# Optimization experiments

Measured on AMD Instinct MI355X. Metric: run time of the kernel, lower is better.

The kernel has to match this reference:

```python
import jax, jax.numpy as jnp
import numpy as np
from jax import lax

THRESHOLD = 0.95
NUM_HEADS = 32
Q_HEAD_DIM = 96
K_DIM = 1024
EPS = 1e-8


def dynamic_token_replacement(emb, thr=THRESHOLD):
    """Greedy sequential merge: token j is replaced by the first earlier
    *unused* token i with cosine sim > thr. emb: (S, D) -> (S, D)."""
    S = emb.shape[0]
    norm = jnp.maximum(jnp.linalg.norm(emb, axis=-1, keepdims=True), EPS)
    n = emb / norm
    sim = n @ n.T  # (S, S) cosine similarity
    idx = jnp.arange(S)

    def step(carry, xs):
        used, rep = carry
        i, row = xs
        # i can only absorb later, unused tokens, and only if i itself is unused
        cand = (idx > i) & (row > thr) & (~used) & (~used[i])
        rep = jnp.where(cand, i, rep)
        used = used | cand
        return (used, rep), None

    (used, rep), _ = lax.scan(step, (jnp.zeros(S, bool), idx), (idx, sim))
    return emb[rep]


def setup_inputs() -> dict:
    key = jax.random.key(0)
    ks = jax.random.split(key, 7)
    B, S, D = 2, 1024, 3072
    s = 0.02
    return {
        "hidden_states": jax.random.normal(ks[0], (B, S, D), jnp.float32),
        "Wq": jax.random.normal(ks[1], (D, D), jnp.float32) * s,
        "bq": jnp.zeros((D,), jnp.float32),
        "Wk": jax.random.normal(ks[2], (D, K_DIM), jnp.float32) * s,
        "bk": jnp.zeros((K_DIM,), jnp.float32),
        "Wv": jax.random.normal(ks[3], (D, K_DIM), jnp.float32) * s,
        "bv": jnp.zeros((K_DIM,), jnp.float32),
        "Wqk": jax.random.normal(ks[4], (Q_HEAD_DIM, K_DIM), jnp.float32) * s,
        "bqk": jnp.zeros((K_DIM,), jnp.float32),
        "Wo": jax.random.normal(ks[5], (K_DIM, D), jnp.float32) * s,
        "bo": jnp.zeros((D,), jnp.float32),
    }


def reference(hidden_states, Wq, bq, Wk, bk, Wv, bv, Wqk, bqk, Wo, bo):
    B, S, D = hidden_states.shape
    q = hidden_states @ Wq + bq                      # (B, S, 3072)
    k = hidden_states @ Wk + bk                      # (B, S, 1024)
    v = hidden_states @ Wv + bv                      # (B, S, 1024)

    q = q.reshape(B, S, NUM_HEADS, Q_HEAD_DIM).transpose(0, 2, 1, 3)  # (B, H, S, 96)
    q_new = q @ Wqk + bqk                            # (B, H, S, 1024)

    new_k = jax.vmap(dynamic_token_replacement)(k)   # (B, S, 1024)
    new_v = jax.vmap(dynamic_token_replacement)(v)   # (B, S, 1024)

    scale = 1.0 / jnp.sqrt(jnp.float32(K_DIM))
    scores = jnp.einsum('bhsk,btk->bhst', q_new, new_k) * scale  # (B, H, S, S)
    attn = jax.nn.softmax(scores, axis=-1)
    out = jnp.einsum('bhst,btk->bhsk', attn, new_v)  # (B, H, S, 1024)
    out = out.mean(axis=1)                           # (B, S, 1024)
    return out @ Wo + bo                             # (B, S, 3072)
```

## Files before the change

kernel.cpp:

```cpp
#include <hip/hip_runtime.h>
#include <hip/hip_bf16.h>
#include <stdint.h>

#define BATCH 2
#define SEQ   1024
#define DIM   3072
#define KDIM  1024
#define NHEAD 32
#define HDQ   96
#define THR_SIM 0.95f

typedef unsigned short u16;
typedef __attribute__((ext_vector_type(8))) short short8;
typedef __attribute__((ext_vector_type(4))) float f32x4;

typedef const __attribute__((address_space(1))) unsigned int* gas_ptr;
typedef __attribute__((address_space(3))) unsigned int* las_ptr;

__device__ __forceinline__ void glds16(const u16* g, u16* l) {
  __builtin_amdgcn_global_load_lds((gas_ptr)g, (las_ptr)l, 16, 0, 0);
}

__device__ __forceinline__ u16 f2bf(float f) {
  union { float f; unsigned u; } v; v.f = f;
  unsigned r = v.u + 0x7FFFu + ((v.u >> 16) & 1u);
  return (u16)(r >> 16);
}
__device__ __forceinline__ float bf2f(u16 x) {
  union { unsigned u; float f; } v; v.u = ((unsigned)x) << 16; return v.f;
}

__device__ __forceinline__ f32x4 mfma16(short8 a, short8 b, f32x4 c) {
  return __builtin_amdgcn_mfma_f32_16x16x32_bf16(a, b, c, 0, 0, 0);
}

__global__ void k_cvt_bf16(const float* __restrict__ in, u16* __restrict__ out, int n4) {
  int i = blockIdx.x * blockDim.x + threadIdx.x;
  if (i < n4) {
    float4 v = ((const float4*)in)[i];
    ushort4 o;
    o.x = f2bf(v.x); o.y = f2bf(v.y); o.z = f2bf(v.z); o.w = f2bf(v.w);
    ((ushort4*)out)[i] = o;
  }
}

__global__ void k_tr_f32_bf16(const float* __restrict__ in, u16* __restrict__ out, int R, int C) {
  __shared__ float t[32][33];
  int c0 = blockIdx.x * 32, r0 = blockIdx.y * 32;
  int tx = threadIdx.x, ty = threadIdx.y;
  #pragma unroll
  for (int k = 0; k < 4; ++k)
    t[ty + 8 * k][tx] = in[(size_t)(r0 + ty + 8 * k) * C + c0 + tx];
  __syncthreads();
  #pragma unroll
  for (int k = 0; k < 4; ++k)
    out[(size_t)(c0 + ty + 8 * k) * R + r0 + tx] = f2bf(t[tx][ty + 8 * k]);
}

__global__ void k_tr_bf16(const u16* __restrict__ in, u16* __restrict__ out,
                          int ldin, int ldout, long long zsIn, long long zsOut) {
  __shared__ u16 t[32][33];
  const u16* ib = in + (size_t)blockIdx.z * zsIn;
  u16* ob = out + (size_t)blockIdx.z * zsOut;
  int c0 = blockIdx.x * 32, r0 = blockIdx.y * 32;
  int tx = threadIdx.x, ty = threadIdx.y;
  #pragma unroll
  for (int k = 0; k < 4; ++k)
    t[ty + 8 * k][tx] = ib[(size_t)(r0 + ty + 8 * k) * ldin + c0 + tx];
  __syncthreads();
  #pragma unroll
  for (int k = 0; k < 4; ++k)
    ob[(size_t)(c0 + ty + 8 * k) * ldout + r0 + tx] = t[tx][ty + 8 * k];
}

__global__ void k_build_wqke(const float* __restrict__ Wqk, const float* __restrict__ bqk,
                             u16* __restrict__ out) {
  const int n = blockIdx.x;
  const int c = threadIdx.x * 4;
  float4 v;
  if (n < 96)       v = *(const float4*)(Wqk + (size_t)n * KDIM + c);
  else if (n == 96) v = *(const float4*)(bqk + c);
  else              v = make_float4(0.f, 0.f, 0.f, 0.f);
  ushort4 o;
  o.x = f2bf(v.x); o.y = f2bf(v.y); o.z = f2bf(v.z); o.w = f2bf(v.w);
  *(ushort4*)(out + (size_t)n * KDIM + c) = o;
}

__global__ void k_bkv(const float* __restrict__ bk, const float* __restrict__ bv,
                      float* __restrict__ out) {
  int i = blockIdx.x * 256 + threadIdx.x;
  if (i < 2048) out[i] = (i < 1024) ? bk[i] : bv[i - 1024];
}

template<bool OUT_BF16, bool BIAS>
__global__ __launch_bounds__(256, 4) void k_gemm_bt(
    const u16* __restrict__ A, const u16* __restrict__ Bt, void* __restrict__ Cv,
    const float* __restrict__ bias, int M, int N, int K,
    int lda, int ldb, int ldc,
    long long bsAH, long long bsAL, long long bsBH, long long bsBL,
    long long bsCH, long long bsCL)
{
  const int zb = blockIdx.y, zH = zb >> 1, zL = zb & 1;
  A  += (size_t)(zH * bsAH + zL * bsAL);
  Bt += (size_t)(zH * bsBH + zL * bsBL);
  u16*   Cb16 = (u16*)Cv + (size_t)(zH * bsCH + zL * bsCL);
  float* Cf32 = (float*)Cv + (size_t)(zH * bsCH + zL * bsCL);

  __shared__ u16 As[2][128 * 32];
  __shared__ u16 Bs[2][64 * 32];
  const int nt = N >> 6;
  const int tm = blockIdx.x / nt, tn = blockIdx.x % nt;
  const int tid = threadIdx.x, lane = tid & 63, wid = tid >> 6;
  const int wr = wid >> 1, wc = wid & 1, li = lane & 15, lg = lane >> 4;

  const int srow = tid >> 2;
  const int scol = (((tid & 3) ^ ((srow >> 1) & 3)) << 3);
  const u16* gA0 = A + (size_t)(tm * 128 + srow) * lda + scol;
  const u16* gA1 = gA0 + (size_t)64 * lda;
  const u16* gB0 = Bt + (size_t)(tn * 64 + srow) * ldb + scol;
  const int wof = wid * 512;

  f32x4 acc[4][2];
  #pragma unroll
  for (int a = 0; a < 4; ++a)
    #pragma unroll
    for (int b = 0; b < 2; ++b) acc[a][b] = (f32x4){0.f, 0.f, 0.f, 0.f};

  const int sl = (lg ^ ((li >> 1) & 3)) * 8;

  const int nk = K >> 5;
  glds16(gA0, As[0] + wof);
  glds16(gA1, As[0] + 2048 + wof);
  glds16(gB0, Bs[0] + wof);
  __syncthreads();

  int cur = 0;
  for (int kt = 0; kt < nk; ++kt) {
    if (kt + 1 < nk) {
      const int k0 = (kt + 1) << 5;
      glds16(gA0 + k0, As[cur ^ 1] + wof);
      glds16(gA1 + k0, As[cur ^ 1] + 2048 + wof);
      glds16(gB0 + k0, Bs[cur ^ 1] + wof);
    }
    short8 af[4], bfv[2];
    #pragma unroll
    for (int mf = 0; mf < 4; ++mf)
      af[mf] = *(const short8*)(As[cur] + (wr * 64 + mf * 16 + li) * 32 + sl);
    #pragma unroll
    for (int nf = 0; nf < 2; ++nf)
      bfv[nf] = *(const short8*)(Bs[cur] + (wc * 32 + nf * 16 + li) * 32 + sl);
    #pragma unroll
    for (int mf = 0; mf < 4; ++mf)
      #pragma unroll
      for (int nf = 0; nf < 2; ++nf)
        acc[mf][nf] = mfma16(af[mf], bfv[nf], acc[mf][nf]);
    __syncthreads();
    cur ^= 1;
  }
  #pragma unroll
  for (int mf = 0; mf < 4; ++mf) {
    #pragma unroll
    for (int nf = 0; nf < 2; ++nf) {
      const int col = tn * 64 + wc * 32 + nf * 16 + li;
      const float bb = BIAS ? bias[col] : 0.f;
      #pragma unroll
      for (int j = 0; j < 4; ++j) {
        const int row = tm * 128 + wr * 64 + mf * 16 + lg * 4 + j;
        const float v = acc[mf][nf][j] + bb;
        if (OUT_BF16) Cb16[(size_t)row * ldc + col] = f2bf(v);
        else          Cf32[(size_t)row * ldc + col] = v;
      }
    }
  }
}

__global__ void k_norms(const float* __restrict__ gram, float* __restrict__ nrm,
                        int* __restrict__ anyCnt) {
  const int s = blockIdx.x, j = threadIdx.x;
  const float* g = gram + (size_t)s * SEQ * SEQ;
  float nj = fmaxf(sqrtf(fmaxf(g[(size_t)j * SEQ + j], 0.f)), 1e-8f);
  nrm[s * SEQ + j] = nj;
  if (j == 0) anyCnt[s] = 0;
}

__global__ void k_rowany(const float* __restrict__ gram, const float* __restrict__ nrm,
                         unsigned char* __restrict__ rowAny, int* __restrict__ anyCnt) {
  const int i = blockIdx.x, s = blockIdx.y, t = threadIdx.x;
  const float* g = gram + (size_t)s * SEQ * SEQ + (size_t)i * SEQ;
  const float* nr = nrm + s * SEQ;
  const float ni = nr[i];
  int any = 0;
  for (int j = i + 1 + t; j < SEQ; j += 256)
    any |= (g[j] > THR_SIM * ni * nr[j]) ? 1 : 0;
  any = __any(any) ? 1 : 0;
  __shared__ int sh[4];
  if ((t & 63) == 0) sh[t >> 6] = any;
  __syncthreads();
  if (t == 0) {
    int a = sh[0] | sh[1] | sh[2] | sh[3];
    rowAny[s * SEQ + i] = (unsigned char)a;
    if (a) atomicAdd(&anyCnt[s], 1);
  }
}

__global__ __launch_bounds__(1024) void k_scan_replace(
    const float* __restrict__ gram, const float* __restrict__ nrmG,
    const unsigned char* __restrict__ rowAnyG, const int* __restrict__ anyCnt,
    u16* __restrict__ kvbase)
{
  const int s = blockIdx.x;
  if (anyCnt[s] == 0) return;
  const float* g = gram + (size_t)s * SEQ * SEQ;
  u16* dat = kvbase + (size_t)(s >> 1) * (2048 * 2048 / 2) * 2 + (size_t)(s & 1) * 1024;
  const int ldr = 2048;
  __shared__ float nrm[SEQ];
  __shared__ unsigned char used[SEQ];
  __shared__ unsigned char rowAny[SEQ];
  __shared__ short rep[SEQ];
  const int j = threadIdx.x;
  nrm[j] = nrmG[s * SEQ + j];
  rowAny[j] = rowAnyG[s * SEQ + j];
  used[j] = 0; rep[j] = (short)j;
  __syncthreads();
  for (int i = 0; i < SEQ - 1; ++i) {
    if (rowAny[i] && !used[i]) {
      const float t = THR_SIM * nrm[i];
      if (j > i && !used[j] && g[(size_t)i * SEQ + j] > t * nrm[j]) {
        used[j] = 1; rep[j] = (short)i;
      }
      __syncthreads();
    }
  }
  __syncthreads();
  const int src = rep[j];
  if (src != j) {
    for (int c = 0; c < KDIM; c += 8)
      *(uint4*)(dat + (size_t)j * ldr + c) = *(const uint4*)(dat + (size_t)src * ldr + c);
  }
}

__global__ __launch_bounds__(1024, 4) void k_attn3(
    const u16* __restrict__ q_bf, const u16* __restrict__ KKTe,
    u16* __restrict__ pbarP)
{
  const int bid = blockIdx.x;
  const int xcd = bid & 7, qt = bid >> 3;
  const int b = xcd >> 2, pg = xcd & 3;
  const int q0 = qt * 16;
  const int tid = threadIdx.x, lane = tid & 63, w = tid >> 6;
  const int li = lane & 15, lg = lane >> 4;

  __shared__ float bkkl[1024];
  __shared__ float2 red[2][16][16];

  const u16* KKb = KKTe + (size_t)b * SEQ * 128;
  bkkl[tid] = bf2f(KKb[(size_t)tid * 128 + 96]);

  short8 ak[4][3];
  #pragma unroll
  for (int kf = 0; kf < 4; ++kf)
    #pragma unroll
    for (int ks = 0; ks < 3; ++ks)
      ak[kf][ks] = *(const short8*)(KKb + (size_t)(w * 64 + kf * 16 + li) * 128 + ks * 32 + lg * 8);

  f32x4 accm[4];
  #pragma unroll
  for (int kf = 0; kf < 4; ++kf) accm[kf] = (f32x4){0.f, 0.f, 0.f, 0.f};
  __syncthreads();

  const u16* qrow = q_bf + (size_t)(b * SEQ + q0 + li) * DIM + pg * 8 * HDQ;

  for (int hh = 0; hh < 8; ++hh) {
    const u16* qp = qrow + hh * HDQ;
    f32x4 acc[4];
    #pragma unroll
    for (int kf = 0; kf < 4; ++kf) acc[kf] = (f32x4){0.f, 0.f, 0.f, 0.f};
    #pragma unroll
    for (int ks = 0; ks < 3; ++ks) {
      short8 bq = *(const short8*)(qp + ks * 32 + lg * 8);
      #pragma unroll
      for (int kf = 0; kf < 4; ++kf)
        acc[kf] = mfma16(ak[kf][ks], bq, acc[kf]);
    }
    float m = -1e30f;
    #pragma unroll
    for (int kf = 0; kf < 4; ++kf) {
      f32x4 bb = *(const f32x4*)(bkkl + w * 64 + kf * 16 + lg * 4);
      #pragma unroll
      for (int j = 0; j < 4; ++j) {
        float s = (acc[kf][j] + bb[j]) * 0.03125f;
        acc[kf][j] = s;
        m = fmaxf(m, s);
      }
    }
    m = fmaxf(m, __shfl_xor(m, 16));
    m = fmaxf(m, __shfl_xor(m, 32));
    float ssum = 0.f;
    #pragma unroll
    for (int kf = 0; kf < 4; ++kf)
      #pragma unroll
      for (int j = 0; j < 4; ++j) {
        float pv = __expf(acc[kf][j] - m);
        acc[kf][j] = pv;
        ssum += pv;
      }
    ssum += __shfl_xor(ssum, 16);
    ssum += __shfl_xor(ssum, 32);
    if (lane < 16) red[hh & 1][w][li] = make_float2(m, ssum);
    __syncthreads();
    float mg = -1e30f;
    #pragma unroll
    for (int ww = 0; ww < 16; ++ww) mg = fmaxf(mg, red[hh & 1][ww][li].x);
    float Sg = 0.f;
    #pragma unroll
    for (int ww = 0; ww < 16; ++ww) {
      float2 msv = red[hh & 1][ww][li];
      Sg += msv.y * __expf(msv.x - mg);
    }
    const float gi = __expf(m - mg) / (32.f * Sg);
    #pragma unroll
    for (int kf = 0; kf < 4; ++kf)
      #pragma unroll
      for (int j = 0; j < 4; ++j)
        accm[kf][j] += acc[kf][j] * gi;
  }

  u16* dst = pbarP + (size_t)(pg * 2 + b) * SEQ * SEQ + (size_t)(q0 + li) * SEQ + w * 64;
  #pragma unroll
  for (int kf = 0; kf < 4; ++kf) {
    ushort4 o;
    o.x = f2bf(accm[kf][0]); o.y = f2bf(accm[kf][1]);
    o.z = f2bf(accm[kf][2]); o.w = f2bf(accm[kf][3]);
    *(ushort4*)(dst + kf * 16 + lg * 4) = o;
  }
}

__global__ void k_reduce_pbar(const u16* __restrict__ part, u16* __restrict__ out) {
  const size_t N = (size_t)BATCH * SEQ * SEQ;
  size_t i = (size_t)blockIdx.x * blockDim.x + threadIdx.x;
  if (i >= N / 8) return;
  short8 p0 = ((const short8*)part)[i];
  short8 p1 = ((const short8*)(part + N))[i];
  short8 p2 = ((const short8*)(part + 2 * N))[i];
  short8 p3 = ((const short8*)(part + 3 * N))[i];
  short8 o;
  #pragma unroll
  for (int j = 0; j < 8; ++j) {
    float s = bf2f((u16)p0[j]) + bf2f((u16)p1[j]) + bf2f((u16)p2[j]) + bf2f((u16)p3[j]);
    o[j] = (short)f2bf(s);
  }
  ((short8*)out)[i] = o;
}

extern "C" void kernel_launch(void* const* d_in, const int* in_sizes, int n_in,
                              void* d_out, int out_size, void* d_ws, size_t ws_size,
                              hipStream_t stream)
{
  (void)in_sizes; (void)n_in; (void)out_size;
  const float* hs  = (const float*)d_in[0];
  const float* Wq  = (const float*)d_in[1];
  const float* bq  = (const float*)d_in[2];
  const float* Wk  = (const float*)d_in[3];
  const float* bk  = (const float*)d_in[4];
  const float* Wv  = (const float*)d_in[5];
  const float* bv  = (const float*)d_in[6];
  const float* Wqk = (const float*)d_in[7];
  const float* bqk = (const float*)d_in[8];
  const float* Wo  = (const float*)d_in[9];
  const float* bo  = (const float*)d_in[10];

  char* p = (char*)d_ws;
  u16*   hs_bf   = (u16*)(p + 0);
  float* gram4   = (float*)(p + 0);
  u16*   pbarP   = (u16*)(p + 0);
  u16*   WqT     = (u16*)(p + 12582912);
  u16*   WkvT    = (u16*)(p + 12582912);
  u16*   WqkE    = (u16*)(p + 16777216);
  u16*   KKTe    = (u16*)(p + 17039360);
  u16*   vTb     = (u16*)(p + 17563648);
  u16*   WoT     = (u16*)(p + 21757952);
  u16*   q_bf    = (u16*)(p + 31457280);
  u16*   kv_bf   = (u16*)(p + 44040192);
  u16*   Pbar_bf = (u16*)(p + 44040192);
  u16*   pv_out  = (u16*)(p + 48234496);
  float* bkv     = (float*)(p + 52428800);
  float* nrm4    = (float*)(p + 52436992);
  unsigned char* rowAny4 = (unsigned char*)(p + 52453376);
  int*   anyCnt  = (int*)(p + 52457472);
  if (ws_size < 58916864) return;

  const dim3 tb(32, 8);
  const long long SS = (long long)SEQ * SEQ;
  const long long KVB = 2048LL * 1024;

  k_cvt_bf16<<<6144, 256, 0, stream>>>(hs, hs_bf, BATCH * SEQ * DIM / 4);
  k_tr_f32_bf16<<<dim3(96, 96), tb, 0, stream>>>(Wq, WqT, DIM, DIM);
  k_gemm_bt<true, true><<<dim3(768, 1), 256, 0, stream>>>(hs_bf, WqT, q_bf, bq,
      2048, DIM, DIM, DIM, DIM, DIM, 0, 0, 0, 0, 0, 0);
  k_tr_f32_bf16<<<dim3(32, 96), tb, 0, stream>>>(Wk, WkvT, DIM, KDIM);
  k_tr_f32_bf16<<<dim3(32, 96), tb, 0, stream>>>(Wv, WkvT + (size_t)1024 * DIM, DIM, KDIM);
  k_bkv<<<8, 256, 0, stream>>>(bk, bv, bkv);
  k_gemm_bt<true, true><<<dim3(512, 1), 256, 0, stream>>>(hs_bf, WkvT, kv_bf, bkv,
      2048, 2048, DIM, DIM, DIM, 2048, 0, 0, 0, 0, 0, 0);
  k_gemm_bt<false, false><<<dim3(128, 4), 256, 0, stream>>>(kv_bf, kv_bf, gram4, nullptr,
      SEQ, SEQ, KDIM, 2048, 2048, SEQ,
      KVB, 1024, KVB, 1024, 2 * SS, SS);
  k_norms<<<4, 1024, 0, stream>>>(gram4, nrm4, anyCnt);
  k_rowany<<<dim3(SEQ, 4), 256, 0, stream>>>(gram4, nrm4, rowAny4, anyCnt);
  k_scan_replace<<<4, 1024, 0, stream>>>(gram4, nrm4, rowAny4, anyCnt, kv_bf);
  k_build_wqke<<<128, 256, 0, stream>>>(Wqk, bqk, WqkE);
  k_gemm_bt<true, false><<<dim3(16, 2), 256, 0, stream>>>(kv_bf, WqkE, KKTe, nullptr,
      SEQ, 128, KDIM, 2048, KDIM, 128, 0, KVB, 0, 0, 0, (long long)SEQ * 128);
  k_tr_bf16<<<dim3(32, 32, 2), tb, 0, stream>>>(kv_bf + 1024, vTb, 2048, SEQ, KVB, SS);
  k_tr_f32_bf16<<<dim3(96, 32), tb, 0, stream>>>(Wo, WoT, KDIM, DIM);
  k_attn3<<<512, 1024, 0, stream>>>(q_bf, KKTe, pbarP);
  k_reduce_pbar<<<1024, 256, 0, stream>>>(pbarP, Pbar_bf);
  k_gemm_bt<true, false><<<dim3(128, 2), 256, 0, stream>>>(Pbar_bf, vTb, pv_out, nullptr,
      SEQ, KDIM, SEQ, SEQ, SEQ, KDIM, 0, SS, 0, SS, 0, SS);
  k_gemm_bt<false, true><<<dim3(768, 1), 256, 0, stream>>>(pv_out, WoT, (float*)d_out, bo,
      2048, DIM, KDIM, KDIM, KDIM, DIM, 0, 0, 0, 0, 0, 0);
}
```

Before: 310.0 us.

## Double GEMM K-tile to 64, remap workgroups across XCDs, new LDS swizzle

The bf16 GEMM kernel now stages a K-slab of 64 instead of 32 per iteration, which halves the number of barriers and loop trips. A new per-8-row XOR swizzle layout goes with it in one unified LDS buffer. Block indices are remapped so that consecutive tiles land on the same XCD (8 chiplets on MI355X), which should improve L2 locality. Shared memory doubles to 48KB per block, so the launch bound drops to 3 blocks per CU. That trades occupancy for fewer syncs and better reuse.

```diff
diff --git a/kernel.cpp b/kernel.cpp
--- a/kernel.cpp
+++ b/kernel.cpp
@@ -93,7 +93,7 @@
 }
 
 template<bool OUT_BF16, bool BIAS>
-__global__ __launch_bounds__(256, 4) void k_gemm_bt(
+__global__ __launch_bounds__(256, 3) void k_gemm_bt(
     const u16* __restrict__ A, const u16* __restrict__ Bt, void* __restrict__ Cv,
     const float* __restrict__ bias, int M, int N, int K,
     int lda, int ldb, int ldc,
@@ -106,19 +106,30 @@
   u16*   Cb16 = (u16*)Cv + (size_t)(zH * bsCH + zL * bsCL);
   float* Cf32 = (float*)Cv + (size_t)(zH * bsCH + zL * bsCL);
 
-  __shared__ u16 As[2][128 * 32];
-  __shared__ u16 Bs[2][64 * 32];
+  __shared__ u16 Ls[2][24 * 512];
   const int nt = N >> 6;
-  const int tm = blockIdx.x / nt, tn = blockIdx.x % nt;
+  int bid = blockIdx.x;
+  {
+    const int nwg = gridDim.x;
+    const int qq = nwg >> 3, rr = nwg & 7;
+    const int x = bid & 7, pos = bid >> 3;
+    bid = (x < rr ? x * (qq + 1) : rr * (qq + 1) + (x - rr) * qq) + pos;
+  }
+  const int tm = bid / nt, tn = bid % nt;
   const int tid = threadIdx.x, lane = tid & 63, wid = tid >> 6;
   const int wr = wid >> 1, wc = wid & 1, li = lane & 15, lg = lane >> 4;
 
-  const int srow = tid >> 2;
-  const int scol = (((tid & 3) ^ ((srow >> 1) & 3)) << 3);
-  const u16* gA0 = A + (size_t)(tm * 128 + srow) * lda + scol;
-  const u16* gA1 = gA0 + (size_t)64 * lda;
-  const u16* gB0 = Bt + (size_t)(tn * 64 + srow) * ldb + scol;
-  const int wof = wid * 512;
+  const int rsub = lane >> 3;
+  const int cbe = ((lane & 7) ^ rsub) << 3;
+  const u16* gp[6];
+  int lof[6];
+  #pragma unroll
+  for (int j = 0; j < 6; ++j) {
+    const int ci = wid * 6 + j;
+    lof[j] = ci << 9;
+    if (ci < 16) gp[j] = A + (size_t)(tm * 128 + ci * 8 + rsub) * lda + cbe;
+    else         gp[j] = Bt + (size_t)(tn * 64 + (ci - 16) * 8 + rsub) * ldb + cbe;
+  }
 
   f32x4 acc[4][2];
   #pragma unroll
@@ -126,36 +137,37 @@
     #pragma unroll
     for (int b = 0; b < 2; ++b) acc[a][b] = (f32x4){0.f, 0.f, 0.f, 0.f};
 
-  const int sl = (lg ^ ((li >> 1) & 3)) * 8;
-
-  const int nk = K >> 5;
-  glds16(gA0, As[0] + wof);
-  glds16(gA1, As[0] + 2048 + wof);
-  glds16(gB0, Bs[0] + wof);
-  __syncthreads();
-
-  int cur = 0;
+  const int nk = K >> 6;
+  #pragma unroll
+  for (int j = 0; j < 6; ++j) { glds16(gp[j], Ls[0] + lof[j]); gp[j] += 64; }
+  __syncthreads();
+
   for (int kt = 0; kt < nk; ++kt) {
+    const u16* Lc = Ls[kt & 1];
     if (kt + 1 < nk) {
-      const int k0 = (kt + 1) << 5;
-      glds16(gA0 + k0, As[cur ^ 1] + wof);
-      glds16(gA1 + k0, As[cur ^ 1] + 2048 + wof);
-      glds16(gB0 + k0, Bs[cur ^ 1] + wof);
-    }
-    short8 af[4], bfv[2];
-    #pragma unroll
-    for (int mf = 0; mf < 4; ++mf)
-      af[mf] = *(const short8*)(As[cur] + (wr * 64 + mf * 16 + li) * 32 + sl);
-    #pragma unroll
-    for (int nf = 0; nf < 2; ++nf)
-      bfv[nf] = *(const short8*)(Bs[cur] + (wc * 32 + nf * 16 + li) * 32 + sl);
-    #pragma unroll
-    for (int mf = 0; mf < 4; ++mf)
+      u16* Ln = Ls[(kt + 1) & 1];
+      #pragma unroll
+      for (int j = 0; j < 6; ++j) { glds16(gp[j], Ln + lof[j]); gp[j] += 64; }
+    }
+    short8 af[2][4], bfv[2][2];
+    #pragma unroll
+    for (int ks = 0; ks < 2; ++ks) {
+      const int sw = (((ks * 4 + lg) ^ (li & 7)) << 3);
+      #pragma unroll
+      for (int mf = 0; mf < 4; ++mf)
+        af[ks][mf] = *(const short8*)(Lc + (wr * 64 + mf * 16 + li) * 64 + sw);
       #pragma unroll
       for (int nf = 0; nf < 2; ++nf)
-        acc[mf][nf] = mfma16(af[mf], bfv[nf], acc[mf][nf]);
+        bfv[ks][nf] = *(const short8*)(Lc + 8192 + (wc * 32 + nf * 16 + li) * 64 + sw);
+    }
+    #pragma unroll
+    for (int ks = 0; ks < 2; ++ks)
+      #pragma unroll
+      for (int mf = 0; mf < 4; ++mf)
+        #pragma unroll
+        for (int nf = 0; nf < 2; ++nf)
+          acc[mf][nf] = mfma16(af[ks][mf], bfv[ks][nf], acc[mf][nf]);
     __syncthreads();
-    cur ^= 1;
   }
   #pragma unroll
   for (int mf = 0; mf < 4; ++mf) {
```

Measured after the change: 251.0 us. 19.0% less time.
